# Performance work log

Measured on AMD Instinct MI355X. Metric: run time of the kernel, lower is better.

Reference implementation:

```python
import jax, jax.numpy as jnp
import numpy as np
from jax import lax

BEAM = 4
MAXLEN = 12
V, E, H = 32000, 256, 512
S, B = 512, 8


def lstm_cell(x, h, c, Wih, Whh, bih, bhh):
    # torch gate order: input, forget, cell, output
    g = x @ Wih.T + h @ Whh.T + bih + bhh
    i, f, gg, o = jnp.split(g, 4, axis=-1)
    c2 = jax.nn.sigmoid(f) * c + jax.nn.sigmoid(i) * jnp.tanh(gg)
    return jax.nn.sigmoid(o) * jnp.tanh(c2), c2


def lstm_layer(xs, Wih, Whh, bih, bhh):
    Bn, Hn = xs.shape[1], Whh.shape[1]
    h0 = jnp.zeros((Bn, Hn), xs.dtype)

    def step(carry, x):
        h, c = carry
        h, c = lstm_cell(x, h, c, Wih, Whh, bih, bhh)
        return (h, c), h

    (hT, cT), hs = lax.scan(step, (h0, h0), xs)
    return hs, hT, cT


def setup_inputs():
    key = jax.random.key(0)
    ks = jax.random.split(key, 32)

    def p(i, shape, s=0.08):
        return jax.random.normal(ks[i], shape, jnp.float32) * s

    return {
        'text': jax.random.randint(ks[0], (S, B), 0, V),
        'emb_enc': p(1, (V, E)),
        'emb_dec': p(2, (V, E)),
        'enc_Wih0': p(3, (4 * H, E)), 'enc_Whh0': p(4, (4 * H, H)),
        'enc_bih0': p(5, (4 * H,)), 'enc_bhh0': p(6, (4 * H,)),
        'enc_Wih1': p(7, (4 * H, H)), 'enc_Whh1': p(8, (4 * H, H)),
        'enc_bih1': p(9, (4 * H,)), 'enc_bhh1': p(10, (4 * H,)),
        'dec_Wih': p(11, (4 * H, E)), 'dec_Whh': p(12, (4 * H, H)),
        'dec_bih': p(13, (4 * H,)), 'dec_bhh': p(14, (4 * H,)),
        'Wq': p(15, (H, H)), 'bq': p(16, (H,)),
        'Wk': p(17, (H, H)), 'bk': p(18, (H,)),
        'Wv': p(19, (H, H)), 'bv': p(20, (H,)),
        'Wo': p(21, (H, H)), 'bo': p(22, (H,)),
        'Wout': p(23, (V, H)), 'bout': p(24, (V,)),
    }


def reference(text, emb_enc, emb_dec, enc_Wih0, enc_Whh0, enc_bih0, enc_bhh0,
              enc_Wih1, enc_Whh1, enc_bih1, enc_bhh1,
              dec_Wih, dec_Whh, dec_bih, dec_bhh,
              Wq, bq, Wk, bk, Wv, bv, Wo, bo, Wout, bout):
    # ---- encoder: 2-layer LSTM over source ----
    emb = emb_enc[text]                                   # [S, B, E]
    hs0, h0, c0 = lstm_layer(emb, enc_Wih0, enc_Whh0, enc_bih0, enc_bhh0)
    hs1, h1, c1 = lstm_layer(hs0, enc_Wih1, enc_Whh1, enc_bih1, enc_bhh1)
    enc_hidden = jnp.stack([h0, h1])                      # [L, B, H] final hidden per layer
    k_enc = enc_hidden @ Wk.T + bk                        # precompute encoder K/V projections
    v_enc = enc_hidden @ Wv.T + bv
    scale = 1.0 / jnp.sqrt(jnp.float32(H))

    # ---- beam state: all beams start from last encoder layer state ----
    dec_h = jnp.tile(h1[None], (BEAM, 1, 1))              # [BEAM, B, H]
    dec_c = jnp.tile(c1[None], (BEAM, 1, 1))
    T = MAXLEN + 1
    result = jnp.full((BEAM, T, B), 1, dtype=jnp.int32)   # SOS token = 1
    logits_hist = jnp.zeros((BEAM, T, B, V), jnp.float32).at[:, 0, :, 1].set(1.0)

    def step(carry, t):
        dh, dc, res, lh = carry
        tok = lax.dynamic_slice(res, (0, t, 0), (BEAM, 1, B))[:, 0, :]      # last token [BEAM, B]
        x = emb_dec[tok]                                                    # [BEAM, B, E]
        nh, nc = lstm_cell(x, dh, dc, dec_Wih, dec_Whh, dec_bih, dec_bhh)   # batched over beams
        # single-head attention: query = dec hidden, keys/values = [enc layers ; dec hidden]
        q = nh @ Wq.T + bq
        kd = nh @ Wk.T + bk
        vd = nh @ Wv.T + bv
        keys = jnp.concatenate([jnp.broadcast_to(k_enc[None], (BEAM,) + k_enc.shape), kd[:, None]], axis=1)  # [BEAM, L+1, B, H]
        vals = jnp.concatenate([jnp.broadcast_to(v_enc[None], (BEAM,) + v_enc.shape), vd[:, None]], axis=1)
        scores = jnp.einsum('nbh,nlbh->nbl', q, keys) * scale
        w = jax.nn.softmax(scores, axis=-1)
        ctx = jnp.einsum('nbl,nlbh->nbh', w, vals)
        dec_out = (ctx @ Wo.T + bo) @ Wout.T + bout                          # [BEAM, B, V]
        # per-beam top-k over vocab, then top-k over the BEAM*BEAM candidates
        pv, pt = lax.top_k(dec_out, BEAM)                                    # [BEAM, B, K]
        cand_v = jnp.transpose(pv, (1, 0, 2)).reshape(B, BEAM * BEAM)        # beam-major blocks
        cand_t = jnp.transpose(pt, (1, 0, 2)).reshape(B, BEAM * BEAM)
        _, ti = lax.top_k(cand_v, BEAM)                                      # [B, K]
        old_beam = (ti // BEAM).T                                            # [BEAM, B]
        new_tok = jnp.take_along_axis(cand_t, ti, axis=1).T                  # [BEAM, B]
        # vectorized beam reorder (gather) of state + history
        nh = jnp.take_along_axis(nh, old_beam[:, :, None], axis=0)
        nc = jnp.take_along_axis(nc, old_beam[:, :, None], axis=0)
        res = jnp.take_along_axis(res, old_beam[:, None, :], axis=0)
        lh = jnp.take_along_axis(lh, old_beam[:, None, :, None], axis=0)
        step_log = jnp.take_along_axis(dec_out, old_beam[:, :, None], axis=0)
        res = lax.dynamic_update_slice(res, new_tok[:, None, :].astype(jnp.int32), (0, t + 1, 0))
        lh = lax.dynamic_update_slice(lh, step_log[:, None], (0, t + 1, 0, 0))
        return (nh, nc, res, lh), None

    (dec_h, dec_c, result, logits_hist), _ = lax.scan(
        step, (dec_h, dec_c, result, logits_hist), jnp.arange(MAXLEN))
    output_res = result[0].T                               # [B, T]
    output_logits = jnp.transpose(logits_hist[0], (1, 2, 0))  # [B, V, T]
    return output_res, output_logits
```

## Files before the change

### kernel.cpp

```cpp
#include <hip/hip_runtime.h>
#include <hip/hip_bf16.h>
#include <float.h>


using ull = unsigned long long;

#define SCOPE_AGENT __HIP_MEMORY_SCOPE_AGENT

__device__ __forceinline__ float cLoad(const float* p) {
  return __hip_atomic_load(p, __ATOMIC_RELAXED, SCOPE_AGENT);
}
__device__ __forceinline__ void cStore(float* p, float v) {
  __hip_atomic_store(p, v, __ATOMIC_RELAXED, SCOPE_AGENT);
}
__device__ __forceinline__ int cLoadI(const int* p) {
  return __hip_atomic_load(p, __ATOMIC_RELAXED, SCOPE_AGENT);
}
__device__ __forceinline__ void cStoreI(int* p, int v) {
  __hip_atomic_store(p, v, __ATOMIC_RELAXED, SCOPE_AGENT);
}
__device__ __forceinline__ ull cLoad64(const ull* p) {
  return __hip_atomic_load(p, __ATOMIC_RELAXED, SCOPE_AGENT);
}
__device__ __forceinline__ void cStore64(ull* p, ull v) {
  __hip_atomic_store(p, v, __ATOMIC_RELAXED, SCOPE_AGENT);
}

__device__ __forceinline__ float2 u2f2(ull u) {
  union { ull u; float2 f; } c; c.u = u; return c.f;
}

__device__ __forceinline__ void fbar2(int* arr, int* bc, int phase) {
  __syncthreads();
  if (threadIdx.x == 0) cStoreI(arr + blockIdx.x * 32, phase);
  if (blockIdx.x == 0) {
    const int* f = arr + threadIdx.x * 32;
    while (cLoadI(f) < phase) {}
    __syncthreads();
    if (threadIdx.x < 32) cStoreI(bc + threadIdx.x * 32, phase);
  } else {
    if (threadIdx.x == 0) {
      const int* f = bc + (blockIdx.x >> 3) * 32;
      while (cLoadI(f) < phase) {}
    }
    __syncthreads();
  }
}

__device__ __forceinline__ float sig_(float x) { return 1.0f / (1.0f + expf(-x)); }

__device__ __forceinline__ void ins4(float* v, int* id, float nv, int ni) {
  if (nv > v[3] || (nv == v[3] && ni < id[3])) {
    v[3] = nv; id[3] = ni;
#pragma unroll
    for (int p = 3; p > 0; --p) {
      bool sw = (v[p] > v[p - 1]) || (v[p] == v[p - 1] && id[p] < id[p - 1]);
      if (sw) {
        float t0 = v[p]; v[p] = v[p - 1]; v[p - 1] = t0;
        int t1 = id[p]; id[p] = id[p - 1]; id[p - 1] = t1;
      }
    }
  }
}

__global__ __launch_bounds__(256) void init_kernel(float* h0buf, float* h1buf,
                                                   int* arrE, int* bcE,
                                                   int* arrD, int* bcD) {
  int g = blockIdx.x * 256 + threadIdx.x;
  if (g < 8192) {
    h0buf[g] = 0.0f; h1buf[g] = 0.0f;
    arrE[g] = 0; arrD[g] = 0;
  }
  if (g < 1024) { bcE[g] = 0; bcD[g] = 0; }
}

struct EncP {
  const int* text; const float* emb;
  const float* Wih0; const float* Whh0; const float* bih0; const float* bhh0;
  const float* Wih1; const float* Whh1; const float* bih1; const float* bhh1;
  float* h0buf; float* h1buf; float* h0f; float* h1f; float* c1f;
  int* arr; int* bc;
};

template <int KX>
__device__ void enc_run(const EncP& P, float* xcat, int w, int tid) {
  constexpr int KTOT = KX + 512;
  constexpr int ST = KTOT + 4;
  constexpr int KSL = KTOT / 8;
  constexpr int Q = KSL / 4;
  constexpr int L = (KX == 512) ? 1 : 0;
  __shared__ float part[16 * 8 * 8];
  __shared__ float gl[128];

  const int c0 = (w & 127) * 4;
  const int kh = tid >> 5, col = (tid >> 3) & 3, b = tid & 7;
  const int kbase = kh * KSL;

  const float* Wih = L ? P.Wih1 : P.Wih0;
  const float* Whh = L ? P.Whh1 : P.Whh0;

  const float4* wih4[4]; const float4* whh4[4];
#pragma unroll
  for (int g = 0; g < 4; ++g) {
    const int row = g * 512 + c0 + col;
    wih4[g] = (const float4*)(Wih + (size_t)row * KX);
    whh4[g] = (const float4*)(Whh + (size_t)row * 512);
  }
  float bsum = 0.f;
  if (tid < 128) {
    const int r = tid >> 3;
    const int row = (r & 3) * 512 + c0 + (r >> 2);
    bsum = (L ? P.bih1[row] + P.bhh1[row] : P.bih0[row] + P.bhh0[row]);
  }
  float creg = 0.f;
  float* myH = L ? P.h1buf : P.h0buf;

  int qx = (KX - kbase) / 4;
  qx = qx < 0 ? 0 : (qx > Q ? Q : qx);

  for (int i = 0; i <= 512; ++i) {
    const bool act = L ? (i >= 1) : (i < 512);
    if (act) {
      const int t = L ? (i - 1) : i;
      if constexpr (KX == 256) {
        for (int e = tid; e < 1024; e += 256) {
          const int b2 = e >> 7, k2 = e & 127;
          const int tokv = P.text[t * 8 + b2];
          float2 v = *(const float2*)(P.emb + (size_t)tokv * 256 + 2 * k2);
          *(float2*)(xcat + b2 * ST + 2 * k2) = v;
        }
      } else {
        const ull* x0 = (const ull*)(P.h0buf + ((i + 1) & 1) * 4096);
        for (int e = tid; e < 2048; e += 256) {
          const int b2 = e >> 8, k2 = e & 255;
          ull u = cLoad64(x0 + b2 * 256 + k2);
          *(ull*)(xcat + b2 * ST + 2 * k2) = u;
        }
      }
      {
        const float* hp = L ? (P.h1buf + (i & 1) * 4096)
                            : (P.h0buf + ((i + 1) & 1) * 4096);
        const ull* hq = (const ull*)hp;
        for (int e = tid; e < 2048; e += 256) {
          const int b2 = e >> 8, k2 = e & 255;
          ull u = cLoad64(hq + b2 * 256 + k2);
          *(ull*)(xcat + b2 * ST + KX + 2 * k2) = u;
        }
      }
      __syncthreads();
      float a0 = 0.f, a1 = 0.f, a2 = 0.f, a3 = 0.f;
      const float4* xq = (const float4*)(xcat + b * ST + kbase);
      const int iw = kbase >> 2, ih = (kbase - KX) >> 2;
#pragma unroll 4
      for (int q = 0; q < qx; ++q) {
        float4 x = xq[q];
        float4 w0 = wih4[0][iw + q], w1 = wih4[1][iw + q];
        float4 w2 = wih4[2][iw + q], w3 = wih4[3][iw + q];
        a0 = fmaf(w0.x, x.x, a0); a0 = fmaf(w0.y, x.y, a0);
        a0 = fmaf(w0.z, x.z, a0); a0 = fmaf(w0.w, x.w, a0);
        a1 = fmaf(w1.x, x.x, a1); a1 = fmaf(w1.y, x.y, a1);
        a1 = fmaf(w1.z, x.z, a1); a1 = fmaf(w1.w, x.w, a1);
        a2 = fmaf(w2.x, x.x, a2); a2 = fmaf(w2.y, x.y, a2);
        a2 = fmaf(w2.z, x.z, a2); a2 = fmaf(w2.w, x.w, a2);
        a3 = fmaf(w3.x, x.x, a3); a3 = fmaf(w3.y, x.y, a3);
        a3 = fmaf(w3.z, x.z, a3); a3 = fmaf(w3.w, x.w, a3);
      }
#pragma unroll 4
      for (int q = qx; q < Q; ++q) {
        float4 x = xq[q];
        float4 w0 = whh4[0][ih + q], w1 = whh4[1][ih + q];
        float4 w2 = whh4[2][ih + q], w3 = whh4[3][ih + q];
        a0 = fmaf(w0.x, x.x, a0); a0 = fmaf(w0.y, x.y, a0);
        a0 = fmaf(w0.z, x.z, a0); a0 = fmaf(w0.w, x.w, a0);
        a1 = fmaf(w1.x, x.x, a1); a1 = fmaf(w1.y, x.y, a1);
        a1 = fmaf(w1.z, x.z, a1); a1 = fmaf(w1.w, x.w, a1);
        a2 = fmaf(w2.x, x.x, a2); a2 = fmaf(w2.y, x.y, a2);
        a2 = fmaf(w2.z, x.z, a2); a2 = fmaf(w2.w, x.w, a2);
        a3 = fmaf(w3.x, x.x, a3); a3 = fmaf(w3.y, x.y, a3);
        a3 = fmaf(w3.z, x.z, a3); a3 = fmaf(w3.w, x.w, a3);
      }
      part[((col * 4 + 0) * 8 + b) * 8 + kh] = a0;
      part[((col * 4 + 1) * 8 + b) * 8 + kh] = a1;
      part[((col * 4 + 2) * 8 + b) * 8 + kh] = a2;
      part[((col * 4 + 3) * 8 + b) * 8 + kh] = a3;
      __syncthreads();
      if (tid < 128) {
        const int r = tid >> 3, b2 = tid & 7;
        const float4* pp = (const float4*)(part + (r * 8 + b2) * 8);
        float4 p0 = pp[0], p1 = pp[1];
        gl[r * 8 + b2] =
            bsum + (((p0.x + p0.y) + (p0.z + p0.w)) + ((p1.x + p1.y) + (p1.z + p1.w)));
      }
      __syncthreads();
      if (tid < 32) {
        const int cc = tid >> 3, b2 = tid & 7;
        float gi = gl[(cc * 4 + 0) * 8 + b2], gf_ = gl[(cc * 4 + 1) * 8 + b2];
        float gg = gl[(cc * 4 + 2) * 8 + b2], go = gl[(cc * 4 + 3) * 8 + b2];
        float c2 = sig_(gf_) * creg + sig_(gi) * tanhf(gg);
        float hv = sig_(go) * tanhf(c2);
        creg = c2;
        cStore(myH + (t & 1) * 4096 + b2 * 512 + c0 + cc, hv);
        if (t == 511) {
          (L ? P.h1f : P.h0f)[b2 * 512 + c0 + cc] = hv;
          if (L) P.c1f[b2 * 512 + c0 + cc] = c2;
        }
      }
    }
    if (i < 512) fbar2(P.arr, P.bc, i + 1);
  }
}

__global__ __launch_bounds__(256, 1) void enc_kernel(EncP P) {
  __shared__ float xcat0[8 * 772];
  __shared__ float xcat1[8 * 1028];
  if (blockIdx.x >> 7) enc_run<512>(P, xcat1, blockIdx.x, threadIdx.x);
  else enc_run<256>(P, xcat0, blockIdx.x, threadIdx.x);
}

__global__ __launch_bounds__(256) void prep_kernel(
    const float* Wk, const float* bk, const float* Wv, const float* bv,
    const float* h0f, const float* h1f, const float* c1f,
    float* kenc, float* venc, float* nhb, float* ncb) {
  const int w = blockIdx.x, tid = threadIdx.x;
  if (w < 64) {
    const int o = w * 256 + tid;
    const int kv = o >> 13, l = (o >> 12) & 1, b = (o >> 9) & 7, c = o & 511;
    const float4* h4 = (const float4*)((l ? h1f : h0f) + b * 512);
    const float4* w4 = (const float4*)((kv ? Wv : Wk) + (size_t)c * 512);
    float s0 = 0.f, s1 = 0.f, s2 = 0.f, s3 = 0.f;
#pragma unroll 8
    for (int k = 0; k < 128; ++k) {
      float4 a = w4[k], x = h4[k];
      s0 = fmaf(a.x, x.x, s0); s1 = fmaf(a.y, x.y, s1);
      s2 = fmaf(a.z, x.z, s2); s3 = fmaf(a.w, x.w, s3);
    }
    (kv ? venc : kenc)[l * 4096 + b * 512 + c] =
        (kv ? bv : bk)[c] + ((s0 + s1) + (s2 + s3));
  } else {
    const int o = (w - 64) * 256 + tid;
    nhb[16384 + o] = h1f[o & 4095];
    ncb[16384 + o] = c1f[o & 4095];
  }
}

__global__ __launch_bounds__(256) void prep2_kernel(
    const float* Wq, const float* Wk, const float* Wv, const float* Wo,
    const float* bq, const float* bk, const float* bv,
    const float* kenc, const float* venc,
    float* At, float* W2, float* u, float* pvec, float* veWo, float* bvo,
    float* sl0, float* sbb) {
  const int w = blockIdx.x, tid = threadIdx.x;
#pragma unroll 1
  for (int sub = 0; sub < 2; ++sub) {
    const int d = 2 * w + sub;
    for (int cc = 0; cc < 2; ++cc) {
      const int c = tid + cc * 256;
      float s0 = 0.f, s1 = 0.f, s2 = 0.f, s3 = 0.f;
      for (int i = 0; i < 512; i += 4) {
        s0 = fmaf(Wk[(i + 0) * 512 + d], Wq[(i + 0) * 512 + c], s0);
        s1 = fmaf(Wk[(i + 1) * 512 + d], Wq[(i + 1) * 512 + c], s1);
        s2 = fmaf(Wk[(i + 2) * 512 + d], Wq[(i + 2) * 512 + c], s2);
        s3 = fmaf(Wk[(i + 3) * 512 + d], Wq[(i + 3) * 512 + c], s3);
      }
      At[(size_t)d * 512 + c] = (s0 + s1) + (s2 + s3);
    }
    for (int cc = 0; cc < 2; ++cc) {
      const int dc = tid + cc * 256;
      float s0 = 0.f, s1 = 0.f, s2 = 0.f, s3 = 0.f;
      const float* wor = Wo + (size_t)d * 512;
      for (int c2 = 0; c2 < 512; c2 += 4) {
        s0 = fmaf(wor[c2 + 0], Wv[(size_t)(c2 + 0) * 512 + dc], s0);
        s1 = fmaf(wor[c2 + 1], Wv[(size_t)(c2 + 1) * 512 + dc], s1);
        s2 = fmaf(wor[c2 + 2], Wv[(size_t)(c2 + 2) * 512 + dc], s2);
        s3 = fmaf(wor[c2 + 3], Wv[(size_t)(c2 + 3) * 512 + dc], s3);
      }
      W2[(size_t)d * 512 + dc] = (s0 + s1) + (s2 + s3);
    }
  }
  if (w == 0) {
    for (int cc = 0; cc < 2; ++cc) {
      const int c = tid + cc * 256;
      float a = 0.f;
      for (int i = 0; i < 512; ++i)
        a += Wq[i * 512 + c] * bk[i] + Wk[i * 512 + c] * bq[i];
      u[c] = a;
    }
  } else if (w <= 32) {
    const int idx = (w - 1) * 256 + tid;
    const int l = idx >> 12, b = (idx >> 9) & 7, c = idx & 511;
    const float* ke = kenc + l * 4096 + b * 512;
    float a = 0.f;
    for (int i = 0; i < 512; ++i) a = fmaf(Wq[i * 512 + c], ke[i], a);
    pvec[idx] = a;
  } else if (w <= 64) {
    const int idx = (w - 33) * 256 + tid;
    const int l = idx >> 12, b = (idx >> 9) & 7, j = idx & 511;
    const float* ve = venc + l * 4096 + b * 512;
    const float* wo = Wo + (size_t)j * 512;
    float a = 0.f;
    for (int c = 0; c < 512; ++c) a = fmaf(wo[c], ve[c], a);
    veWo[idx] = a;
  } else if (w == 65) {
    for (int cc = 0; cc < 2; ++cc) {
      const int j = tid + cc * 256;
      const float* wo = Wo + (size_t)j * 512;
      float a = 0.f;
      for (int c = 0; c < 512; ++c) a = fmaf(wo[c], bv[c], a);
      bvo[j] = a;
    }
  } else if (w == 66) {
    if (tid < 16) {
      const int l = tid >> 3, b = tid & 7;
      const float* ke = kenc + l * 4096 + b * 512;
      float a = 0.f;
      for (int i = 0; i < 512; ++i) a = fmaf(bq[i], ke[i], a);
      sl0[tid] = a;
    } else if (tid == 16) {
      float a = 0.f;
      for (int i = 0; i < 512; ++i) a = fmaf(bq[i], bk[i], a);
      sbb[0] = a;
    }
  }
}

__global__ __launch_bounds__(256) void prep3_kernel(
    const float* Wout, const float* bout, const float* bo, const float* veWo,
    float* E0g, float* E1g, float* bcg) {
  __shared__ float sv[8704];
  const int w = blockIdx.x, tid = threadIdx.x;
  for (int e = tid; e < 8704; e += 256)
    sv[e] = (e < 8192) ? veWo[e] : bo[e - 8192];
  __syncthreads();
  const int cbase = w * 125;
  for (int jj = 0; jj < 9; ++jj) {
    const int idx = jj * 256 + tid;
    if (idx < 2125) {
      const int row = cbase + idx / 17, sel = idx % 17;
      const float4* wr = (const float4*)(Wout + (size_t)row * 512);
      const float4* xv = (const float4*)(sv + (sel < 16 ? sel * 512 : 8192));
      float s0 = 0.f, s1 = 0.f, s2 = 0.f, s3 = 0.f;
#pragma unroll 8
      for (int k = 0; k < 128; ++k) {
        float4 a = wr[k], x = xv[k];
        s0 = fmaf(a.x, x.x, s0); s1 = fmaf(a.y, x.y, s1);
        s2 = fmaf(a.z, x.z, s2); s3 = fmaf(a.w, x.w, s3);
      }
      const float s = (s0 + s1) + (s2 + s3);
      if (sel < 16) (sel < 8 ? E0g : E1g)[(size_t)(sel & 7) * 32000 + row] = s;
      else bcg[row] = s + bout[row];
    }
  }
}

struct DecP {
  const float* emb;
  const float* Wih; const float* Whh; const float* bih; const float* bhh;
  const float* Wout;
  const float* At; const float* W2; const float* u; const float* bvo;
  const float* pvec; const float* sl0; const float* sbb;
  const float* E0g; const float* E1g; const float* bcg;
  float* nhb; float* ncb;
  float* vbuf;
  float* part_s;
  ull* pvp;
  int* obh;
  int* res0;
  __hip_bfloat16* hist;
  int* arr; int* bc;
};

__global__ __launch_bounds__(256, 1) void dec_kernel(DecP P) {
  __shared__ float SM[29312];
  __shared__ float gl[2][4][32];
  __shared__ float slS[32][3];
  __shared__ float wslS[96];
  __shared__ float svv[32][8][4];
  __shared__ int sii[32][8][4];
  __shared__ float rvS[32][4];
  __shared__ int rtS[32][4];
  __shared__ int resS[4][13][8];
  __shared__ int oblS[32];
  __shared__ int tokS[32];
  __shared__ float pscS[32][8];
  __shared__ float nhsS[32][8];

  const int w = blockIdx.x, tid = threadIdx.x;
  float* hs = SM;
  float* tileS = SM;
  float* vqS = SM + 16896;
  float* tvE = SM + 21120;
  int* tiE = (int*)(SM + 25280);
  int ph = 0;

  if (tid < 104) {
    for (int n = 0; n < 4; ++n) resS[n][tid >> 3][tid & 7] = 1;
  }

  auto do_select = [&](int tt) {
    {
      const int r = tid >> 3, ch = tid & 7;
      float m4[4] = {-FLT_MAX, -FLT_MAX, -FLT_MAX, -FLT_MAX};
      int mi[4] = {0x7fffffff, 0x7fffffff, 0x7fffffff, 0x7fffffff};
      for (int g = 0; g < 4; ++g) {
        ull pk[32];
#pragma unroll
        for (int z = 0; z < 32; ++z) {
          const int wg = ch * 32 + g * 8 + (z >> 2);
          pk[z] = cLoad64(P.pvp + wg * 128 + r * 4 + (z & 3));
        }
#pragma unroll
        for (int z = 0; z < 32; ++z)
          ins4(m4, mi, __uint_as_float((unsigned)(pk[z] >> 32)),
               (int)(unsigned)(pk[z] & 0xffffffffu));
      }
#pragma unroll
      for (int k = 0; k < 4; ++k) { svv[r][ch][k] = m4[k]; sii[r][ch][k] = mi[k]; }
    }
    __syncthreads();
    if (tid < 32) {
      float m4[4] = {-FLT_MAX, -FLT_MAX, -FLT_MAX, -FLT_MAX};
      int mi[4] = {0x7fffffff, 0x7fffffff, 0x7fffffff, 0x7fffffff};
      for (int g2 = 0; g2 < 8; ++g2)
#pragma unroll
        for (int k = 0; k < 4; ++k) ins4(m4, mi, svv[tid][g2][k], sii[tid][g2][k]);
#pragma unroll
      for (int k = 0; k < 4; ++k) { rvS[tid][k] = m4[k]; rtS[tid][k] = mi[k]; }
    }
    __syncthreads();
    if (tid < 8) {
      const int b2 = tid;
      unsigned used = 0;
      int obl_[4], tkl_[4];
#pragma unroll
      for (int sel = 0; sel < 4; ++sel) {
        float bestv = -FLT_MAX; int bestj = -1;
        for (int j = 0; j < 16; ++j) {
          if (used & (1u << j)) continue;
          float vv = rvS[(j >> 2) * 8 + b2][j & 3];
          if (vv > bestv) { bestv = vv; bestj = j; }
        }
        used |= 1u << bestj;
        const int obn = bestj >> 2;
        obl_[sel] = obn;
        tkl_[sel] = rtS[obn * 8 + b2][bestj & 3];
        oblS[sel * 8 + b2] = obn;
        tokS[sel * 8 + b2] = tkl_[sel];
        if (w == 0) P.obh[tt * 32 + sel * 8 + b2] = obn;
      }
      if (w == 0) {
        int tmp[4][13];
        for (int n2 = 0; n2 < 4; ++n2)
          for (int s2 = 0; s2 < 13; ++s2) tmp[n2][s2] = resS[obl_[n2]][s2][b2];
        for (int n2 = 0; n2 < 4; ++n2)
          for (int s2 = 0; s2 < 13; ++s2) resS[n2][s2][b2] = tmp[n2][s2];
        for (int n2 = 0; n2 < 4; ++n2) resS[n2][tt + 1][b2] = tkl_[n2];
      }
    }
    __syncthreads();
    if (tt == 11 && w == 0 && tid < 104)
      P.res0[tid] = resS[0][tid >> 3][tid & 7];
  };

  for (int t = 0; t < 12; ++t) {
    const int curOff = (t & 1) * 16384, prevOff = ((t + 1) & 1) * 16384;

    if (t == 0) {
      __syncthreads();
      if (tid < 32) { oblS[tid] = tid >> 3; tokS[tid] = 1; }
      __syncthreads();
    } else {
      do_select(t - 1);
    }
    {
      const int col_l = tid >> 7, gate = (tid >> 5) & 3, nb = tid & 31;
      const int col = 2 * w + col_l;
      const int row = gate * 512 + col;
      for (int e = tid; e < 2048; e += 256) {
        const int nb2 = e >> 6, kf = e & 63;
        float4 v = *((const float4*)(P.emb + (size_t)tokS[nb2] * 256) + kf);
        *((float4*)hs + nb2 * 65 + kf) = v;
      }
      __syncthreads();
      float s0 = 0.f, s1 = 0.f, s2 = 0.f, s3 = 0.f;
      {
        const float4* a4 = (const float4*)(P.Wih + (size_t)row * 256);
        const float4* x4 = (const float4*)hs + nb * 65;
#pragma unroll 8
        for (int k = 0; k < 64; ++k) {
          float4 a = a4[k], x = x4[k];
          s0 = fmaf(a.x, x.x, s0); s1 = fmaf(a.y, x.y, s1);
          s2 = fmaf(a.z, x.z, s2); s3 = fmaf(a.w, x.w, s3);
        }
      }
      float acc = P.bih[row] + P.bhh[row];
      const ull* hsrc = (const ull*)(P.nhb + prevOff);
      const float4* w4row = (const float4*)(P.Whh + (size_t)row * 512);
      for (int ck = 0; ck < 2; ++ck) {
        __syncthreads();
        for (int e = tid; e < 4096; e += 256) {
          const int nb2 = e >> 7, k2 = e & 127;
          const int srow = oblS[nb2] * 8 + (nb2 & 7);
          ull v = cLoad64(hsrc + srow * 256 + ck * 128 + k2);
          *(ull*)(hs + nb2 * 260 + 2 * k2) = v;
        }
        __syncthreads();
        const float4* h4 = (const float4*)hs + nb * 65;
        const float4* w4 = w4row + ck * 64;
#pragma unroll 8
        for (int k = 0; k < 64; ++k) {
          float4 a = w4[k], x = h4[k];
          s0 = fmaf(a.x, x.x, s0); s1 = fmaf(a.y, x.y, s1);
          s2 = fmaf(a.z, x.z, s2); s3 = fmaf(a.w, x.w, s3);
        }
      }
      acc += (s0 + s1) + (s2 + s3);
      gl[col_l][gate][nb] = acc;
      __syncthreads();
      if (tid < 64) {
        const int cc = tid >> 5, nb2 = tid & 31;
        const int col2 = 2 * w + cc;
        float gi = gl[cc][0][nb2], gf_ = gl[cc][1][nb2];
        float gg = gl[cc][2][nb2], go = gl[cc][3][nb2];
        const int srow = oblS[nb2] * 8 + (nb2 & 7);
        float cold = cLoad(P.ncb + prevOff + srow * 512 + col2);
        float c2 = sig_(gf_) * cold + sig_(gi) * tanhf(gg);
        float hv = sig_(go) * tanhf(c2);
        cStore(P.nhb + curOff + nb2 * 512 + col2, hv);
        cStore(P.ncb + curOff + nb2 * 512 + col2, c2);
      }
    }
    fbar2(P.arr, P.bc, ++ph);

    if (w < 128) {
      const int p = w >> 6, cb = w & 63;
      const int col_l = tid >> 5, nb = tid & 31;
      const int col = cb * 8 + col_l;
      const float* W = (p ? P.W2 : P.At) + (size_t)col * 512;
      float acc = (p ? P.bvo : P.u)[col];
      {
        const float4* w4row = (const float4*)W;
        float s0 = 0.f, s1 = 0.f, s2 = 0.f, s3 = 0.f;
        for (int ck = 0; ck < 2; ++ck) {
          __syncthreads();
          const ull* s8 = (const ull*)(P.nhb + curOff);
          for (int e = tid; e < 4096; e += 256) {
            const int nb2 = e >> 7, k2 = e & 127;
            ull v = cLoad64(s8 + nb2 * 256 + ck * 128 + k2);
            *(ull*)(hs + nb2 * 260 + 2 * k2) = v;
          }
          __syncthreads();
          const float4* h4 = (const float4*)hs + nb * 65;
          const float4* w4 = w4row + ck * 64;
#pragma unroll 8
          for (int k = 0; k < 64; ++k) {
            float4 a = w4[k], x = h4[k];
            s0 = fmaf(a.x, x.x, s0); s1 = fmaf(a.y, x.y, s1);
            s2 = fmaf(a.z, x.z, s2); s3 = fmaf(a.w, x.w, s3);
          }
        }
        acc += (s0 + s1) + (s2 + s3);
      }
      if (p) {
        cStore(P.vbuf + nb * 512 + col, acc);
      } else {
        const float nhv = cLoad(P.nhb + curOff + nb * 512 + col);
        pscS[nb][col_l] = nhv * acc;
        nhsS[nb][col_l] = nhv;
        __syncthreads();
        if (tid < 32) {
          const int nb2 = tid, b = nb2 & 7;
          float s2a = 0.f, l0 = 0.f, l1 = 0.f;
#pragma unroll
          for (int i2 = 0; i2 < 8; ++i2) {
            s2a += pscS[nb2][i2];
            const float nv = nhsS[nb2][i2];
            l0 = fmaf(nv, P.pvec[b * 512 + cb * 8 + i2], l0);
            l1 = fmaf(nv, P.pvec[4096 + b * 512 + cb * 8 + i2], l1);
          }
          cStore(P.part_s + (0 * 32 + nb2) * 64 + cb, l0);
          cStore(P.part_s + (1 * 32 + nb2) * 64 + cb, l1);
          cStore(P.part_s + (2 * 32 + nb2) * 64 + cb, s2a);
        }
      }
    }
    fbar2(P.arr, P.bc, ++ph);

    {
      const int cbase = w * 125;
      if (tid < 96) {
        const int nb = tid / 3, l = tid - (tid / 3) * 3, b = nb & 7;
        const ull* ps = (const ull*)(P.part_s + (l * 32 + nb) * 64);
        ull pk[32];
#pragma unroll
        for (int z = 0; z < 32; ++z) pk[z] = cLoad64(ps + z);
        float s = 0.f;
#pragma unroll
        for (int z = 0; z < 32; ++z) { float2 f = u2f2(pk[z]); s += f.x + f.y; }
        const float bias = (l < 2) ? P.sl0[l * 8 + b] : P.sbb[0];
        slS[nb][l] = (s + bias) * (1.0f / sqrtf(512.0f));
      }
      __syncthreads();
      if (tid < 32) {
        float a = slS[tid][0], b2 = slS[tid][1], c3 = slS[tid][2];
        float m = fmaxf(a, fmaxf(b2, c3));
        float e0 = expf(a - m), e1 = expf(b2 - m), e2 = expf(c3 - m);
        float inv = 1.0f / (e0 + e1 + e2);
        wslS[tid * 3 + 0] = e0 * inv;
        wslS[tid * 3 + 1] = e1 * inv;
        wslS[tid * 3 + 2] = e2 * inv;
      }
      const int rg = tid >> 3, ng = tid & 7;
      float acc[4][4];
#pragma unroll
      for (int i = 0; i < 4; ++i)
#pragma unroll
        for (int j = 0; j < 4; ++j) acc[i][j] = 0.f;
      for (int q = 0; q < 4; ++q) {
        __syncthreads();
        for (int e = tid; e < 1024; e += 256) {
          const int nb = e >> 5, kf = e & 31;
          ull u0 = cLoad64((const ull*)(P.vbuf + nb * 512 + q * 128 + kf * 4));
          ull u1 = cLoad64((const ull*)(P.vbuf + nb * 512 + q * 128 + kf * 4 + 2));
          float2 a = u2f2(u0), b2 = u2f2(u1);
          float4 v = {a.x, a.y, b2.x, b2.y};
          *(float4*)(vqS + (nb & 3) * 1056 + (nb >> 2) * 132 + kf * 4) = v;
        }
        for (int it = 0; it < 16; ++it) {
          const int idx = it * 256 + tid;
          if (idx < 4000) {
            const int r = idx >> 5, kf = idx & 31;
            float4 v = *(const float4*)(P.Wout + (size_t)(cbase + r) * 512 +
                                        q * 128 + kf * 4);
            *(float4*)(tileS + (r & 3) * 4224 + (r >> 2) * 132 + kf * 4) = v;
          }
        }
        __syncthreads();
        for (int kf = 0; kf < 32; ++kf) {
          float4 xv[4], wv[4];
#pragma unroll
          for (int j = 0; j < 4; ++j)
            xv[j] = *(const float4*)(vqS + j * 1056 + ng * 132 + kf * 4);
#pragma unroll
          for (int i = 0; i < 4; ++i)
            wv[i] = *(const float4*)(tileS + i * 4224 + rg * 132 + kf * 4);
#pragma unroll
          for (int i = 0; i < 4; ++i)
#pragma unroll
            for (int j = 0; j < 4; ++j) {
              float a = acc[i][j];
              a = fmaf(wv[i].x, xv[j].x, a); a = fmaf(wv[i].y, xv[j].y, a);
              a = fmaf(wv[i].z, xv[j].z, a); a = fmaf(wv[i].w, xv[j].w, a);
              acc[i][j] = a;
            }
        }
      }
      __syncthreads();
      float w0w[4], w1w[4], w2w[4];
#pragma unroll
      for (int j = 0; j < 4; ++j) {
        const int nb = ng * 4 + j;
        w0w[j] = wslS[nb * 3 + 0]; w1w[j] = wslS[nb * 3 + 1]; w2w[j] = wslS[nb * 3 + 2];
      }
      float v4[4][4]; int i4[4][4];
#pragma unroll
      for (int j = 0; j < 4; ++j)
#pragma unroll
        for (int k = 0; k < 4; ++k) { v4[j][k] = -FLT_MAX; i4[j][k] = 0x7fffffff; }
#pragma unroll
      for (int i = 0; i < 4; ++i) {
        const int r = rg * 4 + i;
        if (r < 125) {
          const int c = cbase + r;
          const float bcv = P.bcg[c];
#pragma unroll
          for (int j = 0; j < 4; ++j) {
            const int nb = ng * 4 + j, b = nb & 7;
            const float e0 = P.E0g[(size_t)b * 32000 + c];
            const float e1 = P.E1g[(size_t)b * 32000 + c];
            const float L = fmaf(w2w[j], acc[i][j],
                                 fmaf(w0w[j], e0, fmaf(w1w[j], e1, bcv)));
            P.hist[(size_t)t * 1024000 + (size_t)nb * 32000 + c] = __float2bfloat16(L);
            ins4(v4[j], i4[j], L, c);
          }
        }
      }
#pragma unroll
      for (int j = 0; j < 4; ++j)
#pragma unroll
        for (int k = 0; k < 4; ++k) {
          tvE[(ng * 4 + j) * 130 + rg * 4 + k] = v4[j][k];
          tiE[(ng * 4 + j) * 130 + rg * 4 + k] = i4[j][k];
        }
      __syncthreads();
      if (tid < 32) {
        float m4[4] = {-FLT_MAX, -FLT_MAX, -FLT_MAX, -FLT_MAX};
        int mi[4] = {0x7fffffff, 0x7fffffff, 0x7fffffff, 0x7fffffff};
        for (int e = 0; e < 128; ++e)
          ins4(m4, mi, tvE[tid * 130 + e], tiE[tid * 130 + e]);
#pragma unroll
        for (int k = 0; k < 4; ++k) {
          ull pk = ((ull)__float_as_uint(m4[k]) << 32) | (unsigned)mi[k];
          cStore64(P.pvp + w * 128 + tid * 4 + k, pk);
        }
      }
    }
    fbar2(P.arr, P.bc, ++ph);
  }
  if (w == 0) do_select(11);
}

__global__ __launch_bounds__(256) void out_kernel(const __hip_bfloat16* hist,
                                                  const int* obh, const int* res0,
                                                  float* out) {
  __shared__ float sh[13 * 1000];
  __shared__ int sbArr[12];
  const int w = blockIdx.x, tid = threadIdx.x;
  const int b = w >> 5, v0 = (w & 31) * 1000;
  if (tid == 0) {
    int beta = 0;
    for (int t = 11; t >= 0; --t) {
      const int sb = obh[t * 32 + beta * 8 + b];
      sbArr[t] = sb;
      beta = sb;
    }
  }
  __syncthreads();
  for (int e = tid; e < 12000; e += 256) {
    const int t = e / 1000, vv = e - t * 1000;
    sh[(t + 1) * 1000 + vv] = __bfloat162float(
        hist[(size_t)(t * 32 + sbArr[t] * 8 + b) * 32000 + v0 + vv]);
  }
  for (int e = tid; e < 1000; e += 256) sh[e] = (v0 + e == 1) ? 1.0f : 0.0f;
  __syncthreads();
  float* base = out + 104 + (size_t)(b * 32000 + v0) * 13;
  for (int o = tid; o < 13000; o += 256) {
    const int v = o / 13, t = o - v * 13;
    base[o] = sh[t * 1000 + v];
  }
  if (w == 0 && tid < 104) {
    out[(tid & 7) * 13 + (tid >> 3)] = (float)res0[tid];
  }
}

extern "C" void kernel_launch(void* const* d_in, const int* in_sizes, int n_in,
                              void* d_out, int out_size, void* d_ws, size_t ws_size,
                              hipStream_t stream) {
  const int* text  = (const int*)d_in[0];
  const float* embE = (const float*)d_in[1];
  const float* embD = (const float*)d_in[2];
  const float* Wih0 = (const float*)d_in[3];
  const float* Whh0 = (const float*)d_in[4];
  const float* bih0 = (const float*)d_in[5];
  const float* bhh0 = (const float*)d_in[6];
  const float* Wih1 = (const float*)d_in[7];
  const float* Whh1 = (const float*)d_in[8];
  const float* bih1 = (const float*)d_in[9];
  const float* bhh1 = (const float*)d_in[10];
  const float* dWih = (const float*)d_in[11];
  const float* dWhh = (const float*)d_in[12];
  const float* dbih = (const float*)d_in[13];
  const float* dbhh = (const float*)d_in[14];
  const float* Wq = (const float*)d_in[15];
  const float* bq = (const float*)d_in[16];
  const float* Wk = (const float*)d_in[17];
  const float* bk = (const float*)d_in[18];
  const float* Wv = (const float*)d_in[19];
  const float* bv = (const float*)d_in[20];
  const float* Wo = (const float*)d_in[21];
  const float* bo = (const float*)d_in[22];
  const float* Wout = (const float*)d_in[23];
  const float* bout = (const float*)d_in[24];

  char* ws = (char*)d_ws;
  size_t off = 0;
  auto alloc = [&](size_t bytes) -> char* {
    off = (off + 511) & ~(size_t)511;
    char* p = ws + off;
    off += bytes;
    return p;
  };
  int* arrE  = (int*)alloc(8192 * 4);
  int* bcE   = (int*)alloc(1024 * 4);
  int* arrD  = (int*)alloc(8192 * 4);
  int* bcD   = (int*)alloc(1024 * 4);
  float* h0buf = (float*)alloc(2 * 4096 * 4);
  float* h1buf = (float*)alloc(2 * 4096 * 4);
  float* h0f  = (float*)alloc(4096 * 4);
  float* h1f  = (float*)alloc(4096 * 4);
  float* c1f  = (float*)alloc(4096 * 4);
  float* kenc = (float*)alloc(8192 * 4);
  float* venc = (float*)alloc(8192 * 4);
  float* At   = (float*)alloc((size_t)262144 * 4);
  float* W2   = (float*)alloc((size_t)262144 * 4);
  float* u    = (float*)alloc(512 * 4);
  float* pvec = (float*)alloc(8192 * 4);
  float* veWo = (float*)alloc(8192 * 4);
  float* bvo  = (float*)alloc(512 * 4);
  float* sl0  = (float*)alloc(16 * 4);
  float* sbb  = (float*)alloc(32 * 4);
  float* E0g  = (float*)alloc((size_t)256000 * 4);
  float* E1g  = (float*)alloc((size_t)256000 * 4);
  float* bcg  = (float*)alloc(32000 * 4);
  float* nhb  = (float*)alloc(2 * 16384 * 4);
  float* ncb  = (float*)alloc(2 * 16384 * 4);
  float* vbuf = (float*)alloc(16384 * 4);
  float* part_s = (float*)alloc(6144 * 4);
  ull* pvp    = (ull*)alloc((size_t)32768 * 8);
  int* obh    = (int*)alloc(384 * 4);
  int* res0   = (int*)alloc(104 * 4);
  __hip_bfloat16* hist = (__hip_bfloat16*)alloc((size_t)12288000 * 2);
  if (off > ws_size) return;

  init_kernel<<<32, 256, 0, stream>>>(h0buf, h1buf, arrE, bcE, arrD, bcD);

  EncP ep{text, embE, Wih0, Whh0, bih0, bhh0, Wih1, Whh1, bih1, bhh1,
          h0buf, h1buf, h0f, h1f, c1f, arrE, bcE};
  enc_kernel<<<256, 256, 0, stream>>>(ep);

  prep_kernel<<<128, 256, 0, stream>>>(Wk, bk, Wv, bv, h0f, h1f, c1f, kenc, venc,
                                       nhb, ncb);
  prep2_kernel<<<256, 256, 0, stream>>>(Wq, Wk, Wv, Wo, bq, bk, bv, kenc, venc,
                                        At, W2, u, pvec, veWo, bvo, sl0, sbb);
  prep3_kernel<<<256, 256, 0, stream>>>(Wout, bout, bo, veWo, E0g, E1g, bcg);

  DecP dp{embD, dWih, dWhh, dbih, dbhh, Wout,
          At, W2, u, bvo, pvec, sl0, sbb, E0g, E1g, bcg,
          nhb, ncb, vbuf, part_s, pvp, obh, res0, hist, arrD, bcD};
  dec_kernel<<<256, 256, 0, stream>>>(dp);

  out_kernel<<<256, 256, 0, stream>>>(hist, obh, res0, (float*)d_out);
}
```

Before: 7.085 ms.

## Replace centralized grid barrier with replicated per-producer flags and data broadcast

The encoder no longer uses a two-level grid barrier. Each block writes its hidden outputs into 32 replicated, padded slots and raises per-replica flags, and consumers poll only the flags of the producers they depend on. This lets layer 0 and layer 1 progress without a global barrier each step. The decoder barrier becomes a flat all-to-all flag barrier with no block-0 relay. prep3 now stages Wout tiles in shared memory, some shared-memory strides are padded, and init_kernel is replaced by memsets. The cost is much more flag and data traffic and larger workspace.

```diff
diff --git a/kernel.cpp b/kernel.cpp
--- a/kernel.cpp
+++ b/kernel.cpp
@@ -30,21 +30,15 @@
   union { ull u; float2 f; } c; c.u = u; return c.f;
 }
 
-__device__ __forceinline__ void fbar2(int* arr, int* bc, int phase) {
+__device__ __forceinline__ void fbar1(int* fl, int phase) {
   __syncthreads();
-  if (threadIdx.x == 0) cStoreI(arr + blockIdx.x * 32, phase);
-  if (blockIdx.x == 0) {
-    const int* f = arr + threadIdx.x * 32;
+  if (threadIdx.x < 32)
+    cStoreI(fl + (blockIdx.x * 32 + threadIdx.x) * 32, phase);
+  {
+    const int* f = fl + (threadIdx.x * 32 + (blockIdx.x >> 3)) * 32;
     while (cLoadI(f) < phase) {}
-    __syncthreads();
-    if (threadIdx.x < 32) cStoreI(bc + threadIdx.x * 32, phase);
-  } else {
-    if (threadIdx.x == 0) {
-      const int* f = bc + (blockIdx.x >> 3) * 32;
-      while (cLoadI(f) < phase) {}
-    }
-    __syncthreads();
-  }
+  }
+  __syncthreads();
 }
 
 __device__ __forceinline__ float sig_(float x) { return 1.0f / (1.0f + expf(-x)); }
@@ -63,23 +57,12 @@
   }
 }
 
-__global__ __launch_bounds__(256) void init_kernel(float* h0buf, float* h1buf,
-                                                   int* arrE, int* bcE,
-                                                   int* arrD, int* bcD) {
-  int g = blockIdx.x * 256 + threadIdx.x;
-  if (g < 8192) {
-    h0buf[g] = 0.0f; h1buf[g] = 0.0f;
-    arrE[g] = 0; arrD[g] = 0;
-  }
-  if (g < 1024) { bcE[g] = 0; bcD[g] = 0; }
-}
-
 struct EncP {
   const int* text; const float* emb;
   const float* Wih0; const float* Whh0; const float* bih0; const float* bhh0;
   const float* Wih1; const float* Whh1; const float* bih1; const float* bhh1;
-  float* h0buf; float* h1buf; float* h0f; float* h1f; float* c1f;
-  int* arr; int* bc;
+  float* regD; int* regF;
+  float* h0f; float* h1f; float* c1f;
 };
 
 template <int KX>
@@ -91,14 +74,15 @@
   constexpr int L = (KX == 512) ? 1 : 0;
   __shared__ float part[16 * 8 * 8];
   __shared__ float gl[128];
+  __shared__ float hout[32];
 
   const int c0 = (w & 127) * 4;
   const int kh = tid >> 5, col = (tid >> 3) & 3, b = tid & 7;
   const int kbase = kh * KSL;
+  const int rep = w >> 3;
 
   const float* Wih = L ? P.Wih1 : P.Wih0;
   const float* Whh = L ? P.Whh1 : P.Whh0;
-
   const float4* wih4[4]; const float4* whh4[4];
 #pragma unroll
   for (int g = 0; g < 4; ++g) {
@@ -113,10 +97,13 @@
     bsum = (L ? P.bih1[row] + P.bhh1[row] : P.bih0[row] + P.bhh0[row]);
   }
   float creg = 0.f;
-  float* myH = L ? P.h1buf : P.h0buf;
 
   int qx = (KX - kbase) / 4;
   qx = qx < 0 ? 0 : (qx > Q ? Q : qx);
+
+  for (int e = tid; e < 4096; e += 256)
+    xcat[(e >> 9) * ST + KX + (e & 511)] = 0.f;
+  __syncthreads();
 
   for (int i = 0; i <= 512; ++i) {
     const bool act = L ? (i >= 1) : (i < 512);
@@ -126,25 +113,52 @@
         for (int e = tid; e < 1024; e += 256) {
           const int b2 = e >> 7, k2 = e & 127;
           const int tokv = P.text[t * 8 + b2];
-          float2 v = *(const float2*)(P.emb + (size_t)tokv * 256 + 2 * k2);
-          *(float2*)(xcat + b2 * ST + 2 * k2) = v;
-        }
-      } else {
-        const ull* x0 = (const ull*)(P.h0buf + ((i + 1) & 1) * 4096);
-        for (int e = tid; e < 2048; e += 256) {
-          const int b2 = e >> 8, k2 = e & 255;
-          ull u = cLoad64(x0 + b2 * 256 + k2);
-          *(ull*)(xcat + b2 * ST + 2 * k2) = u;
-        }
-      }
-      {
-        const float* hp = L ? (P.h1buf + (i & 1) * 4096)
-                            : (P.h0buf + ((i + 1) & 1) * 4096);
-        const ull* hq = (const ull*)hp;
-        for (int e = tid; e < 2048; e += 256) {
-          const int b2 = e >> 8, k2 = e & 255;
-          ull u = cLoad64(hq + b2 * 256 + k2);
-          *(ull*)(xcat + b2 * ST + KX + 2 * k2) = u;
+          *(float2*)(xcat + b2 * ST + 2 * k2) =
+              *(const float2*)(P.emb + (size_t)tokv * 256 + 2 * k2);
+        }
+      }
+      if (i >= 1) {
+        {
+          const int s = tid;
+          const bool pollit = (s < 128) || (i >= 2);
+          if (pollit) {
+            const int ps = (s < 128) ? ((i - 1) & 1) : (i & 1);
+            const int* f = P.regF + ((ps * 256 + s) * 32 + rep) * 32;
+            while (cLoadI(f) < i) {}
+          }
+        }
+        __syncthreads();
+        if (L == 0) {
+          const int s2 = tid >> 1, fh = (tid & 1) * 16;
+          const float* base =
+              P.regD + (((size_t)((i - 1) & 1) * 32 + rep) * 32) * 256;
+          float v[16];
+#pragma unroll
+          for (int f2 = 0; f2 < 16; ++f2)
+            v[f2] = cLoad(base + (fh + f2) * 256 + s2);
+#pragma unroll
+          for (int j = 0; j < 4; ++j) {
+            const int b2 = (fh >> 2) + j;
+            float4 q = {v[j * 4 + 0], v[j * 4 + 1], v[j * 4 + 2], v[j * 4 + 3]};
+            *(float4*)&xcat[b2 * ST + KX + 4 * s2] = q;
+          }
+        } else {
+          const int s2 = tid;
+          const bool isH = (s2 >= 128);
+          if (!isH || i >= 2) {
+            const int ps = isH ? (i & 1) : ((i - 1) & 1);
+            const int off = isH ? (512 + 4 * (s2 - 128)) : (4 * s2);
+            const float* base = P.regD + (((size_t)ps * 32 + rep) * 32) * 256;
+            float v[32];
+#pragma unroll
+            for (int f2 = 0; f2 < 32; ++f2) v[f2] = cLoad(base + f2 * 256 + s2);
+#pragma unroll
+            for (int b2 = 0; b2 < 8; ++b2) {
+              float4 q = {v[b2 * 4 + 0], v[b2 * 4 + 1], v[b2 * 4 + 2],
+                          v[b2 * 4 + 3]};
+              *(float4*)&xcat[b2 * ST + off] = q;
+            }
+          }
         }
       }
       __syncthreads();
@@ -199,14 +213,27 @@
         float c2 = sig_(gf_) * creg + sig_(gi) * tanhf(gg);
         float hv = sig_(go) * tanhf(c2);
         creg = c2;
-        cStore(myH + (t & 1) * 4096 + b2 * 512 + c0 + cc, hv);
+        hout[b2 * 4 + cc] = hv;
         if (t == 511) {
           (L ? P.h1f : P.h0f)[b2 * 512 + c0 + cc] = hv;
           if (L) P.c1f[b2 * 512 + c0 + cc] = c2;
         }
       }
-    }
-    if (i < 512) fbar2(P.arr, P.bc, i + 1);
+      __syncthreads();
+      {
+        const int pp2 = L ? ((i - 1) & 1) : (i & 1);
+        const int r = tid >> 3, j = tid & 7;
+        float* base = P.regD + (((size_t)pp2 * 32 + r) * 32) * 256;
+#pragma unroll
+        for (int cc2 = 0; cc2 < 4; ++cc2)
+          cStore(base + (j * 4 + cc2) * 256 + w, hout[j * 4 + cc2]);
+      }
+      __syncthreads();
+      if (tid < 32) {
+        const int pp2 = L ? ((i - 1) & 1) : (i & 1);
+        cStoreI(P.regF + ((pp2 * 256 + w) * 32 + tid) * 32, i + 1);
+      }
+    }
   }
 }
 
@@ -326,28 +353,43 @@
 __global__ __launch_bounds__(256) void prep3_kernel(
     const float* Wout, const float* bout, const float* bo, const float* veWo,
     float* E0g, float* E1g, float* bcg) {
-  __shared__ float sv[8704];
+  __shared__ float sv[16 * 516 + 512];
+  __shared__ float stg[8 * 516];
   const int w = blockIdx.x, tid = threadIdx.x;
-  for (int e = tid; e < 8704; e += 256)
-    sv[e] = (e < 8192) ? veWo[e] : bo[e - 8192];
-  __syncthreads();
+  for (int e = tid; e < 8704; e += 256) {
+    if (e < 8192) sv[(e >> 9) * 516 + (e & 511)] = veWo[e];
+    else sv[16 * 516 + (e - 8192)] = bo[e - 8192];
+  }
   const int cbase = w * 125;
-  for (int jj = 0; jj < 9; ++jj) {
-    const int idx = jj * 256 + tid;
-    if (idx < 2125) {
-      const int row = cbase + idx / 17, sel = idx % 17;
-      const float4* wr = (const float4*)(Wout + (size_t)row * 512);
-      const float4* xv = (const float4*)(sv + (sel < 16 ? sel * 512 : 8192));
-      float s0 = 0.f, s1 = 0.f, s2 = 0.f, s3 = 0.f;
+  for (int tile = 0; tile < 16; ++tile) {
+    const int r0 = tile * 8;
+    __syncthreads();
+    for (int e = tid; e < 1024; e += 256) {
+      const int rr = e >> 7, k4 = e & 127;
+      int row = r0 + rr; if (row > 124) row = 124;
+      *(float4*)&stg[rr * 516 + k4 * 4] =
+          *(const float4*)&Wout[(size_t)(cbase + row) * 512 + k4 * 4];
+    }
+    __syncthreads();
+    if (tid < 136) {
+      const int rr = tid / 17, sel = tid - rr * 17;
+      const int row = r0 + rr;
+      if (row < 125) {
+        const float4* a4 = (const float4*)&stg[rr * 516];
+        const float4* x4 =
+            (const float4*)&sv[sel < 16 ? sel * 516 : 16 * 516];
+        float s0 = 0.f, s1 = 0.f, s2 = 0.f, s3 = 0.f;
 #pragma unroll 8
-      for (int k = 0; k < 128; ++k) {
-        float4 a = wr[k], x = xv[k];
-        s0 = fmaf(a.x, x.x, s0); s1 = fmaf(a.y, x.y, s1);
-        s2 = fmaf(a.z, x.z, s2); s3 = fmaf(a.w, x.w, s3);
-      }
-      const float s = (s0 + s1) + (s2 + s3);
-      if (sel < 16) (sel < 8 ? E0g : E1g)[(size_t)(sel & 7) * 32000 + row] = s;
-      else bcg[row] = s + bout[row];
+        for (int k = 0; k < 128; ++k) {
+          float4 a = a4[k], x = x4[k];
+          s0 = fmaf(a.x, x.x, s0); s1 = fmaf(a.y, x.y, s1);
+          s2 = fmaf(a.z, x.z, s2); s3 = fmaf(a.w, x.w, s3);
+        }
+        const float s = (s0 + s1) + (s2 + s3);
+        const int c = cbase + row;
+        if (sel < 16) (sel < 8 ? E0g : E1g)[(size_t)(sel & 7) * 32000 + c] = s;
+        else bcg[c] = s + bout[c];
+      }
     }
   }
 }
@@ -366,11 +408,11 @@
   int* obh;
   int* res0;
   __hip_bfloat16* hist;
-  int* arr; int* bc;
+  int* fl;
 };
 
 __global__ __launch_bounds__(256, 1) void dec_kernel(DecP P) {
-  __shared__ float SM[29312];
+  __shared__ float SM[29600];
   __shared__ float gl[2][4][32];
   __shared__ float slS[32][3];
   __shared__ float wslS[96];
@@ -389,7 +431,7 @@
   float* tileS = SM;
   float* vqS = SM + 16896;
   float* tvE = SM + 21120;
-  int* tiE = (int*)(SM + 25280);
+  int* tiE = (int*)(SM + 25344);
   int ph = 0;
 
   if (tid < 104) {
@@ -529,7 +571,7 @@
         cStore(P.ncb + curOff + nb2 * 512 + col2, c2);
       }
     }
-    fbar2(P.arr, P.bc, ++ph);
+    fbar1(P.fl, ++ph);
 
     if (w < 128) {
       const int p = w >> 6, cb = w & 63;
@@ -583,7 +625,7 @@
         }
       }
     }
-    fbar2(P.arr, P.bc, ++ph);
+    fbar1(P.fl, ++ph);
 
     {
       const int cbase = w * 125;
@@ -688,15 +730,15 @@
       for (int j = 0; j < 4; ++j)
 #pragma unroll
         for (int k = 0; k < 4; ++k) {
-          tvE[(ng * 4 + j) * 130 + rg * 4 + k] = v4[j][k];
-          tiE[(ng * 4 + j) * 130 + rg * 4 + k] = i4[j][k];
+          tvE[(ng * 4 + j) * 132 + rg * 4 + k] = v4[j][k];
+          tiE[(ng * 4 + j) * 132 + rg * 4 + k] = i4[j][k];
         }
       __syncthreads();
       if (tid < 32) {
         float m4[4] = {-FLT_MAX, -FLT_MAX, -FLT_MAX, -FLT_MAX};
         int mi[4] = {0x7fffffff, 0x7fffffff, 0x7fffffff, 0x7fffffff};
         for (int e = 0; e < 128; ++e)
-          ins4(m4, mi, tvE[tid * 130 + e], tiE[tid * 130 + e]);
+          ins4(m4, mi, tvE[tid * 132 + e], tiE[tid * 132 + e]);
 #pragma unroll
         for (int k = 0; k < 4; ++k) {
           ull pk = ((ull)__float_as_uint(m4[k]) << 32) | (unsigned)mi[k];
@@ -704,7 +746,7 @@
         }
       }
     }
-    fbar2(P.arr, P.bc, ++ph);
+    fbar1(P.fl, ++ph);
   }
   if (w == 0) do_select(11);
 }
@@ -779,12 +821,9 @@
     off += bytes;
     return p;
   };
-  int* arrE  = (int*)alloc(8192 * 4);
-  int* bcE   = (int*)alloc(1024 * 4);
-  int* arrD  = (int*)alloc(8192 * 4);
-  int* bcD   = (int*)alloc(1024 * 4);
-  float* h0buf = (float*)alloc(2 * 4096 * 4);
-  float* h1buf = (float*)alloc(2 * 4096 * 4);
+  float* regD = (float*)alloc((size_t)524288 * 4);
+  int* regF   = (int*)alloc((size_t)524288 * 4);
+  int* decFl  = (int*)alloc((size_t)262144 * 4);
   float* h0f  = (float*)alloc(4096 * 4);
   float* h1f  = (float*)alloc(4096 * 4);
   float* c1f  = (float*)alloc(4096 * 4);
@@ -811,10 +850,11 @@
   __hip_bfloat16* hist = (__hip_bfloat16*)alloc((size_t)12288000 * 2);
   if (off > ws_size) return;
 
-  init_kernel<<<32, 256, 0, stream>>>(h0buf, h1buf, arrE, bcE, arrD, bcD);
+  hipMemsetAsync(regF, 0, (size_t)524288 * 4, stream);
+  hipMemsetAsync(decFl, 0, (size_t)262144 * 4, stream);
 
   EncP ep{text, embE, Wih0, Whh0, bih0, bhh0, Wih1, Whh1, bih1, bhh1,
-          h0buf, h1buf, h0f, h1f, c1f, arrE, bcE};
+          regD, regF, h0f, h1f, c1f};
   enc_kernel<<<256, 256, 0, stream>>>(ep);
 
   prep_kernel<<<128, 256, 0, stream>>>(Wk, bk, Wv, bv, h0f, h1f, c1f, kenc, venc,
@@ -825,7 +865,7 @@
 
   DecP dp{embD, dWih, dWhh, dbih, dbhh, Wout,
           At, W2, u, bvo, pvec, sl0, sbb, E0g, E1g, bcg,
-          nhb, ncb, vbuf, part_s, pvp, obh, res0, hist, arrD, bcD};
+          nhb, ncb, vbuf, part_s, pvp, obh, res0, hist, decFl};
   dec_kernel<<<256, 256, 0, stream>>>(dp);
 
   out_kernel<<<256, 256, 0, stream>>>(hist, obh, res0, (float*)d_out);
```

Result: slower. 8.174 ms (+15.4%).
